# Kernel tuning notes

Hardware: AMD Instinct MI355X
Metric: run time of the kernel (lower is better)

Reference implementation:

```python
import jax, jax.numpy as jnp
import numpy as np

KC = 32      # cluster_num
KS = 3       # kernel_size
AREA = KS * KS
ITERS = 10   # KMeans Lloyd iterations (fixed, deterministic init)


def _unfold3(x):
    # torch nn.Unfold(kernel_size=3, padding=1): feature dim ordered cin-major, area-minor
    b, c, h, w = x.shape
    xp = jnp.pad(x, ((0, 0), (0, 0), (1, 1), (1, 1)))
    cols = jnp.stack([xp[:, :, i:i + h, j:j + w] for i in range(KS) for j in range(KS)], axis=2)  # [b,c,area,h,w]
    return cols.reshape(b, c * AREA, h * w).transpose(0, 2, 1)  # [b, hw, c*area]


def _kmeans_assign(feat):
    # Lloyd's KMeans on [s, d] features; deterministic strided init; returns [s] int assignments
    s, d = feat.shape
    c0 = feat[jnp.arange(KC) * (s // KC)]
    f2 = (feat * feat).sum(-1, keepdims=True)
    def dists(c):
        return f2 - 2.0 * feat @ c.T + (c * c).sum(-1)[None, :]
    def step(c, _):
        idx = jnp.argmin(dists(c), axis=1)
        cnt = jax.ops.segment_sum(jnp.ones((s,), feat.dtype), idx, KC)
        sm = jax.ops.segment_sum(feat, idx, KC)
        c_new = jnp.where(cnt[:, None] > 0, sm / jnp.maximum(cnt, 1.0)[:, None], c)
        return c_new, None
    c, _ = jax.lax.scan(step, c0, None, length=ITERS)
    return jnp.argmin(dists(c), axis=1)


def _seg_mean(p, idx):
    # per-cluster mean of patches -> patch-space centroids [K, f]
    s = p.shape[0]
    cnt = jax.ops.segment_sum(jnp.ones((s,), p.dtype), idx, KC)
    return jax.ops.segment_sum(p, idx, KC) / jnp.maximum(cnt, 1.0)[:, None]


def _mlp2(x, W1, b1, W2, b2):
    return jax.nn.relu(jax.nn.relu(x @ W1 + b1) @ W2 + b2)


def setup_inputs():
    key = jax.random.key(0)
    ks = jax.random.split(key, 16)
    cin, cout, m = 32, 32, 16
    f = cin * AREA
    g = lambda k, shp, sc: jax.random.normal(k, shp, dtype=jnp.float32) * sc
    return {
        "x": g(ks[0], (4, cin, 64, 64), 1.0),
        "Wh1": g(ks[1], (f, m), (2.0 / f) ** 0.5), "bh1": jnp.zeros((m,), jnp.float32),
        "Wh2": g(ks[2], (m, m), (2.0 / m) ** 0.5), "bh2": jnp.zeros((m,), jnp.float32),
        "Wa": g(ks[3], (m, AREA), (2.0 / m) ** 0.5), "ba": jnp.zeros((AREA,), jnp.float32),
        "Wc": g(ks[4], (m, cin), (2.0 / m) ** 0.5), "bc": jnp.zeros((cin,), jnp.float32),
        "Wo": g(ks[5], (m, cout), (2.0 / m) ** 0.5), "bo": jnp.zeros((cout,), jnp.float32),
        "kernels": g(ks[6], (cin, AREA, cout), (2.0 / (cin * AREA)) ** 0.5),
        "Wb1": g(ks[7], (f, m), (2.0 / f) ** 0.5), "bb1": jnp.zeros((m,), jnp.float32),
        "Wb2": g(ks[8], (m, m), (2.0 / m) ** 0.5), "bb2": jnp.zeros((m,), jnp.float32),
        "Wb3": g(ks[9], (m, cout), (2.0 / m) ** 0.5), "bb3": jnp.zeros((cout,), jnp.float32),
    }


def reference(x, Wh1, bh1, Wh2, bh2, Wa, ba, Wc, bc, Wo, bo, kernels, Wb1, bb1, Wb2, bb2, Wb3, bb3):
    b, cin, h, w = x.shape
    s = h * w
    cout = kernels.shape[-1]
    patches = _unfold3(x)                                        # [b, s, cin*area]
    feat = patches.reshape(b, s, cin, AREA).mean(-1)             # cluster_source='channel'
    idx = jax.vmap(_kmeans_assign)(jax.lax.stop_gradient(feat))  # [b, s] cluster assignments
    centroids = jax.vmap(_seg_mean)(patches, idx)                # [b, K, cin*area]
    # low_rank kernel generator: rank-1 modulation along cin/area/cout of shared base kernel
    kf = _mlp2(centroids, Wh1, bh1, Wh2, bh2)                    # [b, K, m]
    w_cin = jax.nn.sigmoid(kf @ Wc + bc)                         # [b, K, cin]
    w_area = jax.nn.sigmoid(kf @ Wa + ba)                        # [b, K, area]
    w_cout = jax.nn.sigmoid(kf @ Wo + bo)                        # [b, K, cout]
    kern = (w_cin[:, :, :, None, None] * w_area[:, :, None, :, None]
            * w_cout[:, :, None, None, :] * kernels[None, None])  # [b, K, cin, area, cout]
    kern = kern.reshape(b, KC, cin * AREA, cout)
    bias = _mlp2(centroids, Wb1, bb1, Wb2, bb2) @ Wb3 + bb3      # [b, K, cout] (bias='cluster')
    # gather per-pixel kernel/bias by cluster id, grouped matmul, scatter back (dense-gather form)
    bi = jnp.arange(b)[:, None]
    Wpix = kern[bi, idx]                                         # [b, s, f, cout]
    out = jnp.einsum('bsf,bsfo->bso', patches, Wpix) + bias[bi, idx]
    return out.reshape(b, h, w, cout).transpose(0, 3, 1, 2), idx
```

## Files before the change

kernel.cpp:

```cpp
#include <hip/hip_runtime.h>
#include <stdint.h>

typedef unsigned long long u64;

#define Bn 4
#define CINn 32
#define Hn 64
#define Wn 64
#define Sn 4096
#define KCn 32
#define Mn 16
#define COUTn 32
#define AREAn 9
#define Fn 288
#define NITER 10
#define FXSCALE 4294967296.0
#define NBLK_B 16
#define PXB 256
#define CMAX 160
#define LDK 292
#define NFLAG ((NITER + 2) * Bn * NBLK_B)

#define AT_LD_U32(p)    __hip_atomic_load((p),  __ATOMIC_RELAXED, __HIP_MEMORY_SCOPE_AGENT)
#define AT_LD_U64(p)    __hip_atomic_load((p),  __ATOMIC_RELAXED, __HIP_MEMORY_SCOPE_AGENT)
#define AT_ST_U32(p,v)  __hip_atomic_store((p), (v), __ATOMIC_RELAXED, __HIP_MEMORY_SCOPE_AGENT)
#define AT_ST_U64(p,v)  __hip_atomic_store((p), (v), __ATOMIC_RELAXED, __HIP_MEMORY_SCOPE_AGENT)

static __device__ __forceinline__ float relu_(float v){ return v > 0.f ? v : 0.f; }
static __device__ __forceinline__ float sigmoid_(float v){ return 1.f / (1.f + expf(-v)); }

__global__ __launch_bounds__(256) void k_init(const float* __restrict__ x,
                                              float* __restrict__ feat,
                                              u64* __restrict__ gsum,
                                              unsigned* __restrict__ gcnt,
                                              unsigned* __restrict__ flags){
    int g = blockIdx.x * 256 + threadIdx.x;
    if (g < 3 * Bn * KCn * CINn) gsum[g] = 0ull;
    if (g < 3 * Bn * KCn)        gcnt[g] = 0u;
    if (g < NFLAG)               flags[g] = 0u;
    int p = g & (Sn - 1);
    int c = (g >> 12) & (CINn - 1);
    int b = g >> 17;
    int y = p >> 6, xx = p & 63;
    const float* xc = x + ((size_t)(b * CINn + c) << 12);
    float s = 0.f;
    #pragma unroll
    for (int i = 0; i < 3; ++i){
        int yy = y + i - 1;
        if (yy < 0 || yy >= Hn) continue;
        #pragma unroll
        for (int j = 0; j < 3; ++j){
            int xj = xx + j - 1;
            if (xj < 0 || xj >= Wn) continue;
            s += xc[(yy << 6) + xj];
        }
    }
    feat[g] = s * (1.f / 9.f);
}

struct AssignSh {
    float4 fvQ[8][PXB];
    float  f2L[PXB];
    float4 cent4[KCn][8];
    float  c2[KCn];
    float  bestdM[4][PXB];
    int    bestkM[4][PXB];
    unsigned lcnt[KCn];
    unsigned off32[KCn + 1];
    unsigned scat[KCn];
    unsigned cntPrev[KCn];
    int   plist[PXB];
    int   rankF[PXB];
    unsigned baseBT[KCn];
};
struct SmkSh {
    float psum[CINn][AREAn][8];
    float centL[Fn];
    int   pl[256];
    float part1[16][16], part2[16][16];
    float hL[2][Mn];
    float kfL[2][Mn];
};
union ShU { AssignSh a; SmkSh m; };

__global__ __launch_bounds__(256) void k_main(const float* __restrict__ x,
        const float* __restrict__ feat,
        u64* __restrict__ gsum, unsigned* __restrict__ gcnt,
        unsigned* __restrict__ blkcnt,
        int* __restrict__ idx, float* __restrict__ idxf,
        int* __restrict__ sorted, int4* __restrict__ chunk_map,
        const float* __restrict__ Wh1, const float* __restrict__ bh1,
        const float* __restrict__ Wh2, const float* __restrict__ bh2,
        const float* __restrict__ Wa,  const float* __restrict__ ba,
        const float* __restrict__ Wc,  const float* __restrict__ bc,
        const float* __restrict__ Wo,  const float* __restrict__ bo,
        const float* __restrict__ Wb1, const float* __restrict__ bb1,
        const float* __restrict__ Wb2, const float* __restrict__ bb2,
        const float* __restrict__ Wb3, const float* __restrict__ bb3,
        float* __restrict__ wcin, float* __restrict__ warea,
        float* __restrict__ wcout, float* __restrict__ biasb,
        unsigned* __restrict__ flg){
    __shared__ int bi256[PXB];
    __shared__ unsigned totK[KCn];
    __shared__ unsigned goffK[KCn + 1];
    __shared__ ShU sh;

    const int tid  = threadIdx.x;
    const int b    = blockIdx.x >> 4;
    const int tnum = blockIdx.x & 15;
    const int p    = tnum * PXB + tid;
    const int kq   = tid >> 6;
    const int pxb  = tid & 63;

    #pragma unroll
    for (int cq = 0; cq < 8; ++cq){
        float4 v;
        v.x = feat[(b * CINn + cq * 4 + 0) * Sn + p];
        v.y = feat[(b * CINn + cq * 4 + 1) * Sn + p];
        v.z = feat[(b * CINn + cq * 4 + 2) * Sn + p];
        v.w = feat[(b * CINn + cq * 4 + 3) * Sn + p];
        sh.a.fvQ[cq][tid] = v;
    }
    __syncthreads();
    {
        float s = 0.f;
        #pragma unroll
        for (int cq = 0; cq < 8; ++cq){
            float4 v = sh.a.fvQ[cq][tid];
            s = fmaf(v.x, v.x, s); s = fmaf(v.y, v.y, s);
            s = fmaf(v.z, v.z, s); s = fmaf(v.w, v.w, s);
        }
        sh.a.f2L[tid] = s;
    }

    for (int iter = 0; iter <= NITER; ++iter){
        const int prev = (iter + 2) % 3;
        const int cur  = iter % 3;
        const int nxt  = (iter + 1) % 3;

        if (iter == 0){
            float* centf = (float*)sh.a.cent4;
            for (int e = tid; e < KCn * CINn; e += 256){
                int k = e >> 5, c = e & 31;
                centf[k * 32 + c] = feat[(b * CINn + c) * Sn + k * (Sn / KCn)];
            }
        } else {
            if (tid < NBLK_B)
                while (AT_LD_U32(&flg[(iter - 1) * Bn * NBLK_B + b * NBLK_B + tid]) == 0u)
                    __builtin_amdgcn_s_sleep(2);
            __syncthreads();
            if (tid < KCn)
                sh.a.cntPrev[tid] = AT_LD_U32(&gcnt[(prev * Bn + b) * KCn + tid]);
            u64 sv[4];
            #pragma unroll
            for (int q = 0; q < 4; ++q)
                sv[q] = AT_LD_U64(&gsum[(size_t)(prev * Bn + b) * KCn * CINn + tid + q * 256]);
            __syncthreads();
            float* centf = (float*)sh.a.cent4;
            #pragma unroll
            for (int q = 0; q < 4; ++q){
                int e = tid + q * 256;
                int k = e >> 5, c = e & 31;
                unsigned cn = sh.a.cntPrev[k];
                if (cn > 0)
                    centf[k * 32 + c] = (float)((double)(long long)sv[q] / ((double)cn * FXSCALE));
            }
        }
        if (iter < NITER && tnum == 0){
            for (int e = tid; e < KCn * CINn; e += 256)
                AT_ST_U64(&gsum[(size_t)(nxt * Bn + b) * KCn * CINn + e], 0ull);
            if (tid < KCn) AT_ST_U32(&gcnt[(nxt * Bn + b) * KCn + tid], 0u);
        }
        __syncthreads();
        if (tid < KCn){
            const float4* cr = sh.a.cent4[tid];
            float s = 0.f;
            #pragma unroll
            for (int cq2 = 0; cq2 < 8; ++cq2){
                float4 v = cr[cq2];
                s = fmaf(v.x, v.x, s); s = fmaf(v.y, v.y, s);
                s = fmaf(v.z, v.z, s); s = fmaf(v.w, v.w, s);
            }
            sh.a.c2[tid] = s;
            sh.a.lcnt[tid] = 0u;
            sh.a.scat[tid] = 0u;
        }
        __syncthreads();

        float dot[4][8];
        #pragma unroll
        for (int j = 0; j < 4; ++j)
            #pragma unroll
            for (int kk = 0; kk < 8; ++kk) dot[j][kk] = 0.f;
        #pragma unroll
        for (int cq2 = 0; cq2 < 8; ++cq2){
            float4 fr0 = sh.a.fvQ[cq2][pxb];
            float4 fr1 = sh.a.fvQ[cq2][pxb + 64];
            float4 fr2 = sh.a.fvQ[cq2][pxb + 128];
            float4 fr3 = sh.a.fvQ[cq2][pxb + 192];
            #pragma unroll
            for (int kk = 0; kk < 8; ++kk){
                float4 cv = sh.a.cent4[kq * 8 + kk][cq2];
                dot[0][kk] = fmaf(fr0.x, cv.x, dot[0][kk]); dot[0][kk] = fmaf(fr0.y, cv.y, dot[0][kk]);
                dot[0][kk] = fmaf(fr0.z, cv.z, dot[0][kk]); dot[0][kk] = fmaf(fr0.w, cv.w, dot[0][kk]);
                dot[1][kk] = fmaf(fr1.x, cv.x, dot[1][kk]); dot[1][kk] = fmaf(fr1.y, cv.y, dot[1][kk]);
                dot[1][kk] = fmaf(fr1.z, cv.z, dot[1][kk]); dot[1][kk] = fmaf(fr1.w, cv.w, dot[1][kk]);
                dot[2][kk] = fmaf(fr2.x, cv.x, dot[2][kk]); dot[2][kk] = fmaf(fr2.y, cv.y, dot[2][kk]);
                dot[2][kk] = fmaf(fr2.z, cv.z, dot[2][kk]); dot[2][kk] = fmaf(fr2.w, cv.w, dot[2][kk]);
                dot[3][kk] = fmaf(fr3.x, cv.x, dot[3][kk]); dot[3][kk] = fmaf(fr3.y, cv.y, dot[3][kk]);
                dot[3][kk] = fmaf(fr3.z, cv.z, dot[3][kk]); dot[3][kk] = fmaf(fr3.w, cv.w, dot[3][kk]);
            }
        }
        #pragma unroll
        for (int j = 0; j < 4; ++j){
            const int px = pxb + 64 * j;
            const float f2v = sh.a.f2L[px];
            float bd = 3.402823466e38f; int bkk = kq * 8;
            #pragma unroll
            for (int kk = 0; kk < 8; ++kk){
                float d = f2v - 2.f * dot[j][kk] + sh.a.c2[kq * 8 + kk];
                if (d < bd){ bd = d; bkk = kq * 8 + kk; }
            }
            sh.a.bestdM[kq][px] = bd;
            sh.a.bestkM[kq][px] = bkk;
        }
        __syncthreads();
        int bk;
        {
            float bd = sh.a.bestdM[0][tid]; bk = sh.a.bestkM[0][tid];
            #pragma unroll
            for (int q = 1; q < 4; ++q){
                float d2 = sh.a.bestdM[q][tid];
                if (d2 < bd){ bd = d2; bk = sh.a.bestkM[q][tid]; }
            }
            bi256[tid] = bk;
        }

        if (iter < NITER){
            atomicAdd(&sh.a.lcnt[bk], 1u);
            __syncthreads();
            if (tid == 0){
                unsigned acc = 0;
                #pragma unroll
                for (int k = 0; k < KCn; ++k){ sh.a.off32[k] = acc; acc += sh.a.lcnt[k]; }
                sh.a.off32[KCn] = acc;
            }
            __syncthreads();
            {
                unsigned pos = sh.a.off32[bk] + atomicAdd(&sh.a.scat[bk], 1u);
                sh.a.plist[pos] = tid;
            }
            __syncthreads();
            {
                const int wv   = tid >> 6;
                const int lane = tid & 63;
                const int hf   = lane >> 5;
                const int c    = lane & 31;
                const float* fvf = (const float*)sh.a.fvQ;
                #pragma unroll
                for (int kq2 = 0; kq2 < 8; ++kq2){
                    const int k  = wv * 8 + kq2;
                    const int o0 = (int)sh.a.off32[k];
                    const int n  = (int)sh.a.off32[k + 1] - o0;
                    u64 acc = 0ull;
                    for (int i = hf; i < n; i += 2){
                        int px = sh.a.plist[o0 + i];
                        float fvv = fvf[(c >> 2) * 1024 + px * 4 + (c & 3)];
                        acc += (u64)llrint((double)fvv * FXSCALE);
                    }
                    acc += __shfl_down(acc, 32);
                    if (lane < 32 && n > 0)
                        atomicAdd(&gsum[(size_t)(cur * Bn + b) * KCn * CINn + k * CINn + c], acc);
                }
            }
            if (tid < KCn){
                unsigned v = sh.a.lcnt[tid];
                if (v) atomicAdd(&gcnt[(cur * Bn + b) * KCn + tid], v);
            }
            __syncthreads();
            if (tid == 0)
                AT_ST_U32(&flg[iter * Bn * NBLK_B + b * NBLK_B + tnum], 1u);
        } else {
            idx [b * Sn + p] = bk;
            idxf[b * Sn + p] = (float)bk;
            __syncthreads();
            if (tid < KCn){
                int r = 0;
                for (int q = 0; q < PXB; ++q)
                    if (bi256[q] == tid) sh.a.rankF[q] = r++;
                AT_ST_U32(&blkcnt[(b * KCn + tid) * NBLK_B + tnum], (unsigned)r);
            }
            __syncthreads();
            if (tid == 0)
                AT_ST_U32(&flg[NITER * Bn * NBLK_B + b * NBLK_B + tnum], 1u);
        }
    }

    if (tid < NBLK_B)
        while (AT_LD_U32(&flg[NITER * Bn * NBLK_B + b * NBLK_B + tid]) == 0u)
            __builtin_amdgcn_s_sleep(2);
    __syncthreads();
    if (tid < KCn){
        unsigned run = 0, mybase = 0;
        #pragma unroll 4
        for (int blk = 0; blk < NBLK_B; ++blk){
            unsigned v = AT_LD_U32(&blkcnt[(b * KCn + tid) * NBLK_B + blk]);
            if (blk == tnum) mybase = run;
            run += v;
        }
        totK[tid] = run;
        sh.a.baseBT[tid] = mybase;
    }
    __syncthreads();
    if (tid == 0){
        unsigned acc = 0;
        #pragma unroll
        for (int k = 0; k < KCn; ++k){ goffK[k] = acc; acc += totK[k]; }
        goffK[KCn] = acc;
    }
    __syncthreads();
    {
        int k = bi256[tid];
        unsigned pos = goffK[k] + sh.a.baseBT[k] + (unsigned)sh.a.rankF[tid];
        AT_ST_U32((unsigned*)&sorted[b * Sn + pos], (unsigned)p);
    }
    if (tnum == 0 && tid == 0){
        int j = 0;
        for (int k = 0; k < KCn; ++k){
            int n = (int)totK[k];
            for (int cb = 0; cb < n; cb += 32){
                chunk_map[b * CMAX + j] = make_int4(k, (int)goffK[k] + cb, min(32, n - cb), 0);
                ++j;
            }
        }
        for (; j < CMAX; ++j) chunk_map[b * CMAX + j] = make_int4(-1, 0, 0, 0);
    }
    __syncthreads();
    if (tid == 0)
        AT_ST_U32(&flg[(NITER + 1) * Bn * NBLK_B + b * NBLK_B + tnum], 1u);
    if (tid < NBLK_B)
        while (AT_LD_U32(&flg[(NITER + 1) * Bn * NBLK_B + b * NBLK_B + tid]) == 0u)
            __builtin_amdgcn_s_sleep(2);
    __syncthreads();

    for (int kq2 = 0; kq2 < 2; ++kq2){
        const int kk   = tnum * 2 + kq2;
        const int off0 = (int)goffK[kk];
        const int nmy  = (int)totK[kk];
        __syncthreads();
        {
            const int cA = tid >> 3;
            const int s  = tid & 7;
            const float* xc = x + ((size_t)(b * CINn + cA) << 12);
            float acc[9];
            #pragma unroll
            for (int a = 0; a < 9; ++a) acc[a] = 0.f;
            for (int base = 0; base < nmy; base += 256){
                int m = min(256, nmy - base);
                __syncthreads();
                if (tid < m)
                    sh.m.pl[tid] = (int)AT_LD_U32((unsigned*)&sorted[b * Sn + off0 + base + tid]);
                __syncthreads();
                #pragma unroll 2
                for (int i = s; i < m; i += 8){
                    int pp = sh.m.pl[i];
                    int py = pp >> 6, px2 = pp & 63;
                    #pragma unroll
                    for (int a = 0; a < 9; ++a){
                        int y1 = py + a / 3 - 1, x1 = px2 + (a % 3) - 1;
                        float v = (y1 >= 0 && y1 < Hn && x1 >= 0 && x1 < Wn)
                                  ? xc[(y1 << 6) + x1] : 0.f;
                        acc[a] += v;
                    }
                }
            }
            __syncthreads();
            #pragma unroll
            for (int a = 0; a < 9; ++a) sh.m.psum[cA][a][s] = acc[a];
            __syncthreads();
            float invn = 1.f / (float)max(nmy, 1);
            for (int f = tid; f < Fn; f += 256){
                int c = f / 9, a = f - c * 9;
                float sm = 0.f;
                #pragma unroll
                for (int s2 = 0; s2 < 8; ++s2) sm += sh.m.psum[c][a][s2];
                sh.m.centL[f] = sm * invn;
            }
        }
        __syncthreads();
        {
            int j = tid & 15, rep = tid >> 4;
            float p1 = 0.f, p2 = 0.f;
            int fbeg = rep * 18;
            for (int ff = fbeg; ff < fbeg + 18; ++ff){
                float cv = sh.m.centL[ff];
                p1 = fmaf(cv, Wh1[ff * Mn + j], p1);
                p2 = fmaf(cv, Wb1[ff * Mn + j], p2);
            }
            sh.m.part1[rep][j] = p1;
            sh.m.part2[rep][j] = p2;
        }
        __syncthreads();
        if (tid < 32){
            int br = tid >> 4, j = tid & 15;
            float s = br ? bb1[j] : bh1[j];
            for (int r = 0; r < 16; ++r) s += br ? sh.m.part2[r][j] : sh.m.part1[r][j];
            sh.m.hL[br][j] = relu_(s);
        }
        __syncthreads();
        if (tid < 32){
            int br = tid >> 4, j = tid & 15;
            const float* W2 = br ? Wb2 : Wh2;
            float s = br ? bb2[j] : bh2[j];
            #pragma unroll
            for (int i = 0; i < Mn; ++i) s = fmaf(sh.m.hL[br][i], W2[i * Mn + j], s);
            sh.m.kfL[br][j] = relu_(s);
        }
        __syncthreads();
        if (tid < 32){
            int o = tid;
            float s1 = bc[o], s2 = bo[o], s3 = bb3[o];
            #pragma unroll
            for (int i = 0; i < Mn; ++i){
                float kv = sh.m.kfL[0][i];
                s1 = fmaf(kv, Wc[i * COUTn + o], s1);
                s2 = fmaf(kv, Wo[i * COUTn + o], s2);
                s3 = fmaf(sh.m.kfL[1][i], Wb3[i * COUTn + o], s3);
            }
            wcin [(b * KCn + kk) * CINn  + o] = sigmoid_(s1);
            wcout[(b * KCn + kk) * COUTn + o] = sigmoid_(s2);
            biasb[(b * KCn + kk) * COUTn + o] = s3;
        } else if (tid < 41){
            int a2 = tid - 32;
            float s = ba[a2];
            #pragma unroll
            for (int i = 0; i < Mn; ++i) s = fmaf(sh.m.kfL[0][i], Wa[i * AREAn + a2], s);
            warea[(b * KCn + kk) * AREAn + a2] = sigmoid_(s);
        }
    }
}

__global__ __launch_bounds__(256) void k_out(const float* __restrict__ x,
                                             const int* __restrict__ sorted,
                                             const int4* __restrict__ chunk_map,
                                             const float* __restrict__ wcin,
                                             const float* __restrict__ warea,
                                             const float* __restrict__ wcout,
                                             const float* __restrict__ biasb,
                                             const float* __restrict__ kern0,
                                             float* __restrict__ out){
    const int b   = blockIdx.x / CMAX;
    const int j   = blockIdx.x - b * CMAX;
    const int tid = threadIdx.x;

    int4 cm = chunk_map[b * CMAX + j];
    const int kcur = cm.x;
    if (kcur < 0) return;
    const int base = cm.y;
    const int cnt  = cm.z;

    __shared__ float kernT[COUTn * LDK];
    __shared__ float patchL[32 * LDK];
    __shared__ int   pix[32];
    __shared__ float wcl[CINn], wal[AREAn], wol[COUTn], biasL[COUTn];

    if (tid < 32){
        pix[tid] = (tid < cnt) ? sorted[b * Sn + base + tid] : -1;
    } else if (tid < 64)  wcl[tid - 32]    = wcin [(b * KCn + kcur) * CINn  + tid - 32];
    else if (tid < 96)    wol[tid - 64]    = wcout[(b * KCn + kcur) * COUTn + tid - 64];
    else if (tid < 105)   wal[tid - 96]    = warea[(b * KCn + kcur) * AREAn + tid - 96];
    else if (tid >= 128 && tid < 160) biasL[tid - 128] = biasb[(b * KCn + kcur) * COUTn + tid - 128];

    const int fA = tid;       const int cA = fA / 9, aA = fA - cA * 9;
    const int dyA = aA / 3 - 1, dxA = aA % 3 - 1;
    const int fB = 256 + tid; const int cB = fB / 9, aB = fB - cB * 9;
    const int dyB = aB / 3 - 1, dxB = aB % 3 - 1;
    __syncthreads();

    {
        int o  = tid >> 3;
        int q  = tid & 7;
        int f0 = q * 36;
        int cc = q * 4, aa = 0;
        float wo_ = wol[o];
        float* kr = kernT + o * LDK + f0;
        #pragma unroll 4
        for (int i2 = 0; i2 < 36; ++i2){
            kr[i2] = wcl[cc] * wal[aa] * wo_ * kern0[(f0 + i2) * COUTn + o];
            if (++aa == 9){ aa = 0; ++cc; }
        }
    }

    #pragma unroll 4
    for (int px = 0; px < 32; ++px){
        int pp = pix[px];
        float vA = 0.f, vB = 0.f;
        if (pp >= 0){
            int py = pp >> 6, pxx = pp & 63;
            int y1 = py + dyA, x1 = pxx + dxA;
            if (y1 >= 0 && y1 < Hn && x1 >= 0 && x1 < Wn)
                vA = x[((size_t)(b * CINn + cA) << 12) + (y1 << 6) + x1];
            if (tid < 32){
                int y2 = py + dyB, x2 = pxx + dxB;
                if (y2 >= 0 && y2 < Hn && x2 >= 0 && x2 < Wn)
                    vB = x[((size_t)(b * CINn + cB) << 12) + (y2 << 6) + x2];
            }
        }
        patchL[px * LDK + tid] = vA;
        if (tid < 32) patchL[px * LDK + 256 + tid] = vB;
    }
    __syncthreads();

    const int o2 = tid & 15, p2 = tid >> 4;
    const int oA = o2 * 2, oB = o2 * 2 + 1;
    const int pxA = p2 * 2, pxB = p2 * 2 + 1;
    const bool actA = pxA < cnt, actB = pxB < cnt;
    if (!actA && !actB) return;

    const float* krA = kernT + oA * LDK;
    const float* krB = kernT + oB * LDK;
    const float* prA = patchL + pxA * LDK;
    const float* prB = patchL + pxB * LDK;
    float s00 = 0.f, s01 = 0.f, s10 = 0.f, s11 = 0.f;
    #pragma unroll 4
    for (int fq = 0; fq < Fn; fq += 4){
        float4 k0 = *reinterpret_cast<const float4*>(krA + fq);
        float4 k1 = *reinterpret_cast<const float4*>(krB + fq);
        float4 pa = *reinterpret_cast<const float4*>(prA + fq);
        float4 pb = *reinterpret_cast<const float4*>(prB + fq);
        s00 = fmaf(pa.x,k0.x,s00); s00 = fmaf(pa.y,k0.y,s00); s00 = fmaf(pa.z,k0.z,s00); s00 = fmaf(pa.w,k0.w,s00);
        s01 = fmaf(pa.x,k1.x,s01); s01 = fmaf(pa.y,k1.y,s01); s01 = fmaf(pa.z,k1.z,s01); s01 = fmaf(pa.w,k1.w,s01);
        s10 = fmaf(pb.x,k0.x,s10); s10 = fmaf(pb.y,k0.y,s10); s10 = fmaf(pb.z,k0.z,s10); s10 = fmaf(pb.w,k0.w,s10);
        s11 = fmaf(pb.x,k1.x,s11); s11 = fmaf(pb.y,k1.y,s11); s11 = fmaf(pb.z,k1.z,s11); s11 = fmaf(pb.w,k1.w,s11);
    }
    if (actA){
        int pp = pix[pxA];
        out[((size_t)(b * COUTn + oA) << 12) + pp] = biasL[oA] + s00;
        out[((size_t)(b * COUTn + oB) << 12) + pp] = biasL[oB] + s01;
    }
    if (actB){
        int pp = pix[pxB];
        out[((size_t)(b * COUTn + oA) << 12) + pp] = biasL[oA] + s10;
        out[((size_t)(b * COUTn + oB) << 12) + pp] = biasL[oB] + s11;
    }
}

extern "C" void kernel_launch(void* const* d_in, const int* in_sizes, int n_in,
                              void* d_out, int out_size, void* d_ws, size_t ws_size,
                              hipStream_t stream){
    const float* x    = (const float*)d_in[0];
    const float* Wh1  = (const float*)d_in[1];
    const float* bh1  = (const float*)d_in[2];
    const float* Wh2  = (const float*)d_in[3];
    const float* bh2  = (const float*)d_in[4];
    const float* Wa   = (const float*)d_in[5];
    const float* ba   = (const float*)d_in[6];
    const float* Wc   = (const float*)d_in[7];
    const float* bc   = (const float*)d_in[8];
    const float* Wo   = (const float*)d_in[9];
    const float* bo   = (const float*)d_in[10];
    const float* kern0= (const float*)d_in[11];
    const float* Wb1  = (const float*)d_in[12];
    const float* bb1  = (const float*)d_in[13];
    const float* Wb2  = (const float*)d_in[14];
    const float* bb2  = (const float*)d_in[15];
    const float* Wb3  = (const float*)d_in[16];
    const float* bb3  = (const float*)d_in[17];

    char* ws = (char*)d_ws;
    float*    feat   = (float*)(ws + 0);
    u64*      gsum   = (u64*)  (ws + 2097152);
    unsigned* gcnt   = (unsigned*)(ws + 2195456);
    unsigned* blkcnt = (unsigned*)(ws + 2196992);
    int*      idx    = (int*)  (ws + 2205184);
    int*      sorted = (int*)  (ws + 2270720);
    float*    wcin   = (float*)(ws + 2336256);
    float*    warea  = (float*)(ws + 2352640);
    float*    wcout  = (float*)(ws + 2357248);
    float*    biasb  = (float*)(ws + 2373632);
    int4*     chunk_map = (int4*)(ws + 2390016);
    unsigned* flags  = (unsigned*)(ws + 2400256);

    float* outp = (float*)d_out;
    float* idxf = outp + (size_t)Bn * COUTn * Sn;

    k_init<<<(Bn * CINn * Sn) / 256, 256, 0, stream>>>(x, feat, gsum, gcnt, flags);
    k_main<<<Bn * NBLK_B, 256, 0, stream>>>(x, feat, gsum, gcnt, blkcnt, idx, idxf,
                                            sorted, chunk_map,
                                            Wh1, bh1, Wh2, bh2, Wa, ba, Wc, bc, Wo, bo,
                                            Wb1, bb1, Wb2, bb2, Wb3, bb3,
                                            wcin, warea, wcout, biasb, flags);
    k_out<<<Bn * CMAX, 256, 0, stream>>>(x, sorted, chunk_map, wcin, warea, wcout,
                                         biasb, kern0, outp);
}
```

Before: 230.9 us.

## Pad feature LDS rows, parallelize chunk map, drop idx buffer, remap output tiles

Pads the shared feature array by one float4 per row to reduce LDS bank conflicts in the cluster-sum gather. Keeps per-pixel features in registers for the norm computation, removing one barrier. Removes the unused int idx store and parallelizes chunk_map construction across threads instead of a single serial thread. Changes the output kernel's thread-to-(pixel,channel) mapping from interleaved to strided halves, which alters LDS access patterns. The register array adds pressure in the persistent main kernel.

```diff
diff --git a/kernel.cpp b/kernel.cpp
--- a/kernel.cpp
+++ b/kernel.cpp
@@ -59,7 +59,7 @@
 }
 
 struct AssignSh {
-    float4 fvQ[8][PXB];
+    float4 fvQ[8][PXB + 1];
     float  f2L[PXB];
     float4 cent4[KCn][8];
     float  c2[KCn];
@@ -87,7 +87,7 @@
         const float* __restrict__ feat,
         u64* __restrict__ gsum, unsigned* __restrict__ gcnt,
         unsigned* __restrict__ blkcnt,
-        int* __restrict__ idx, float* __restrict__ idxf,
+        float* __restrict__ idxf,
         int* __restrict__ sorted, int4* __restrict__ chunk_map,
         const float* __restrict__ Wh1, const float* __restrict__ bh1,
         const float* __restrict__ Wh2, const float* __restrict__ bh2,
@@ -103,6 +103,7 @@
     __shared__ int bi256[PXB];
     __shared__ unsigned totK[KCn];
     __shared__ unsigned goffK[KCn + 1];
+    __shared__ unsigned chunkOff[KCn + 1];
     __shared__ ShU sh;
 
     const int tid  = threadIdx.x;
@@ -112,6 +113,7 @@
     const int kq   = tid >> 6;
     const int pxb  = tid & 63;
 
+    float fv[CINn];
     #pragma unroll
     for (int cq = 0; cq < 8; ++cq){
         float4 v;
@@ -120,18 +122,16 @@
         v.z = feat[(b * CINn + cq * 4 + 2) * Sn + p];
         v.w = feat[(b * CINn + cq * 4 + 3) * Sn + p];
         sh.a.fvQ[cq][tid] = v;
-    }
-    __syncthreads();
+        fv[cq * 4 + 0] = v.x; fv[cq * 4 + 1] = v.y;
+        fv[cq * 4 + 2] = v.z; fv[cq * 4 + 3] = v.w;
+    }
     {
         float s = 0.f;
         #pragma unroll
-        for (int cq = 0; cq < 8; ++cq){
-            float4 v = sh.a.fvQ[cq][tid];
-            s = fmaf(v.x, v.x, s); s = fmaf(v.y, v.y, s);
-            s = fmaf(v.z, v.z, s); s = fmaf(v.w, v.w, s);
-        }
+        for (int c = 0; c < CINn; ++c) s = fmaf(fv[c], fv[c], s);
         sh.a.f2L[tid] = s;
     }
+    __syncthreads();
 
     for (int iter = 0; iter <= NITER; ++iter){
         const int prev = (iter + 2) % 3;
@@ -142,7 +142,7 @@
             float* centf = (float*)sh.a.cent4;
             for (int e = tid; e < KCn * CINn; e += 256){
                 int k = e >> 5, c = e & 31;
-                centf[k * 32 + c] = feat[(b * CINn + c) * Sn + k * (Sn / KCn)];
+                centf[e] = feat[(b * CINn + c) * Sn + k * (Sn / KCn)];
             }
         } else {
             if (tid < NBLK_B)
@@ -154,21 +154,20 @@
             u64 sv[4];
             #pragma unroll
             for (int q = 0; q < 4; ++q)
-                sv[q] = AT_LD_U64(&gsum[(size_t)(prev * Bn + b) * KCn * CINn + tid + q * 256]);
+                sv[q] = AT_LD_U64(&gsum[(size_t)(prev * Bn + b) * 1024 + tid + q * 256]);
             __syncthreads();
             float* centf = (float*)sh.a.cent4;
             #pragma unroll
             for (int q = 0; q < 4; ++q){
-                int e = tid + q * 256;
-                int k = e >> 5, c = e & 31;
-                unsigned cn = sh.a.cntPrev[k];
+                const int e = tid + q * 256;
+                unsigned cn = sh.a.cntPrev[e >> 5];
                 if (cn > 0)
-                    centf[k * 32 + c] = (float)((double)(long long)sv[q] / ((double)cn * FXSCALE));
+                    centf[e] = (float)((double)(long long)sv[q] / ((double)cn * FXSCALE));
             }
         }
         if (iter < NITER && tnum == 0){
             for (int e = tid; e < KCn * CINn; e += 256)
-                AT_ST_U64(&gsum[(size_t)(nxt * Bn + b) * KCn * CINn + e], 0ull);
+                AT_ST_U64(&gsum[(size_t)(nxt * Bn + b) * 1024 + e], 0ull);
             if (tid < KCn) AT_ST_U32(&gcnt[(nxt * Bn + b) * KCn + tid], 0u);
         }
         __syncthreads();
@@ -265,12 +264,12 @@
                     u64 acc = 0ull;
                     for (int i = hf; i < n; i += 2){
                         int px = sh.a.plist[o0 + i];
-                        float fvv = fvf[(c >> 2) * 1024 + px * 4 + (c & 3)];
+                        float fvv = fvf[(c >> 2) * 1028 + px * 4 + (c & 3)];
                         acc += (u64)llrint((double)fvv * FXSCALE);
                     }
                     acc += __shfl_down(acc, 32);
                     if (lane < 32 && n > 0)
-                        atomicAdd(&gsum[(size_t)(cur * Bn + b) * KCn * CINn + k * CINn + c], acc);
+                        atomicAdd(&gsum[(size_t)(cur * Bn + b) * 1024 + k * 32 + c], acc);
                 }
             }
             if (tid < KCn){
@@ -281,7 +280,6 @@
             if (tid == 0)
                 AT_ST_U32(&flg[iter * Bn * NBLK_B + b * NBLK_B + tnum], 1u);
         } else {
-            idx [b * Sn + p] = bk;
             idxf[b * Sn + p] = (float)bk;
             __syncthreads();
             if (tid < KCn){
@@ -324,16 +322,22 @@
         unsigned pos = goffK[k] + sh.a.baseBT[k] + (unsigned)sh.a.rankF[tid];
         AT_ST_U32((unsigned*)&sorted[b * Sn + pos], (unsigned)p);
     }
-    if (tnum == 0 && tid == 0){
-        int j = 0;
-        for (int k = 0; k < KCn; ++k){
-            int n = (int)totK[k];
-            for (int cb = 0; cb < n; cb += 32){
-                chunk_map[b * CMAX + j] = make_int4(k, (int)goffK[k] + cb, min(32, n - cb), 0);
-                ++j;
-            }
-        }
-        for (; j < CMAX; ++j) chunk_map[b * CMAX + j] = make_int4(-1, 0, 0, 0);
+    if (tnum == 0){
+        if (tid == 0){
+            unsigned acc = 0;
+            #pragma unroll
+            for (int k = 0; k < KCn; ++k){ chunkOff[k] = acc; acc += (totK[k] + 31) >> 5; }
+            chunkOff[KCn] = acc;
+        }
+        __syncthreads();
+        if (tid < KCn){
+            int n = (int)totK[tid];
+            unsigned j0 = chunkOff[tid];
+            for (int cb = 0; cb < n; cb += 32)
+                chunk_map[b * CMAX + (j0++)] = make_int4(tid, (int)goffK[tid] + cb, min(32, n - cb), 0);
+        }
+        for (int j = (int)chunkOff[KCn] + tid; j < CMAX; j += 256)
+            chunk_map[b * CMAX + j] = make_int4(-1, 0, 0, 0);
     }
     __syncthreads();
     if (tid == 0)
@@ -512,8 +516,8 @@
     __syncthreads();
 
     const int o2 = tid & 15, p2 = tid >> 4;
-    const int oA = o2 * 2, oB = o2 * 2 + 1;
-    const int pxA = p2 * 2, pxB = p2 * 2 + 1;
+    const int oA = o2, oB = o2 + 16;
+    const int pxA = p2, pxB = p2 + 16;
     const bool actA = pxA < cnt, actB = pxB < cnt;
     if (!actA && !actB) return;
 
@@ -568,24 +572,23 @@
     const float* bb3  = (const float*)d_in[17];
 
     char* ws = (char*)d_ws;
-    float*    feat   = (float*)(ws + 0);
-    u64*      gsum   = (u64*)  (ws + 2097152);
-    unsigned* gcnt   = (unsigned*)(ws + 2195456);
-    unsigned* blkcnt = (unsigned*)(ws + 2196992);
-    int*      idx    = (int*)  (ws + 2205184);
-    int*      sorted = (int*)  (ws + 2270720);
-    float*    wcin   = (float*)(ws + 2336256);
-    float*    warea  = (float*)(ws + 2352640);
-    float*    wcout  = (float*)(ws + 2357248);
-    float*    biasb  = (float*)(ws + 2373632);
-    int4*     chunk_map = (int4*)(ws + 2390016);
-    unsigned* flags  = (unsigned*)(ws + 2400256);
+    float*    feat    = (float*)(ws + 0);
+    u64*      gsum    = (u64*)  (ws + 2097152);
+    unsigned* gcnt    = (unsigned*)(ws + 2195456);
+    unsigned* blkcnt  = (unsigned*)(ws + 2196992);
+    int*      sorted  = (int*)  (ws + 2205184);
+    float*    wcin    = (float*)(ws + 2270720);
+    float*    warea   = (float*)(ws + 2287104);
+    float*    wcout   = (float*)(ws + 2291712);
+    float*    biasb   = (float*)(ws + 2308096);
+    int4*     chunk_map = (int4*)(ws + 2324480);
+    unsigned* flags   = (unsigned*)(ws + 2334720);
 
     float* outp = (float*)d_out;
     float* idxf = outp + (size_t)Bn * COUTn * Sn;
 
     k_init<<<(Bn * CINn * Sn) / 256, 256, 0, stream>>>(x, feat, gsum, gcnt, flags);
-    k_main<<<Bn * NBLK_B, 256, 0, stream>>>(x, feat, gsum, gcnt, blkcnt, idx, idxf,
+    k_main<<<Bn * NBLK_B, 256, 0, stream>>>(x, feat, gsum, gcnt, blkcnt, idxf,
                                             sorted, chunk_map,
                                             Wh1, bh1, Wh2, bh2, Wa, ba, Wc, bc, Wo, bo,
                                             Wb1, bb1, Wb2, bb2, Wb3, bb3,
```

New measurement: 217.8 us (median of 2 runs). -5.6%, faster.
